# Kernel optimization log

Hardware: AMD Instinct MI355X
Metric: run time of the kernel (lower is better)

The kernel has to match this reference:

```python
import jax, jax.numpy as jnp
import numpy as np


def setup_inputs() -> dict:
    key = jax.random.key(0)
    k1, k2, k3 = jax.random.split(key, 3)
    B, C = 8192, 10000
    inp = jax.random.normal(k1, (B, C), dtype=jnp.float32)
    distance_matrix = jax.random.uniform(k2, (C, C), dtype=jnp.float32)
    target = jax.random.randint(k3, (B,), 0, C, dtype=jnp.int64)
    return {"input": inp, "distance_matrix": distance_matrix, "target": target}


def reference(input, distance_matrix, target):
    B = input.shape[0]
    C = distance_matrix.shape[0]
    # vectorized replacement for the per-sample narrow+cat loop: row gather
    distance_vector = distance_matrix[target]  # [B, C]
    # NOTE: original uses log_softmax over dim=0 (batch dim) here — faithful.
    log_sm_batch = jax.nn.log_softmax(input, axis=0)  # [B, C]
    inclusive_reg = -0.5 * jnp.sum(distance_vector * log_sm_batch) / (C * B)
    # standard cross entropy (softmax over class dim, mean over batch)
    log_sm_cls = jax.nn.log_softmax(input, axis=1)  # [B, C]
    ce = -jnp.mean(jnp.take_along_axis(log_sm_cls, target[:, None], axis=1))
    return ce + inclusive_reg
```

## Files before the change

### kernel.cpp

```cpp
#include <hip/hip_runtime.h>

#define B_DIM 8192
#define C_DIM 10000
#define C4    2500
#define NT    10
#define TILE4 256
#define NCHUNK 128
#define ROWCHUNK (B_DIM / NCHUNK)
#define NCH2  32

typedef float v4f __attribute__((ext_vector_type(4)));

__global__ __launch_bounds__(256) void fused_main(
    const v4f* __restrict__ x4, const v4f* __restrict__ dm4,
    const int* __restrict__ target,
    v4f* __restrict__ colExpPart, v4f* __restrict__ colDPart,
    float* __restrict__ rowPartExp, float* __restrict__ rowPartDx,
    float* __restrict__ xt) {
    const int tile  = blockIdx.x;
    const int chunk = blockIdx.y;
    const int tid   = threadIdx.x;
    const int lane  = tid & 63;
    const int wave  = tid >> 6;
    const int base4 = tile * TILE4;
    const int row0  = chunk * ROWCHUNK;

    __shared__ int s_t[ROWCHUNK];
    __shared__ v4f sE[TILE4];
    __shared__ v4f sD[TILE4];

    for (int r = tid; r < ROWCHUNK; r += 256) s_t[r] = target[row0 + r];
    __syncthreads();

    int  col4[4];
    bool valid[4];
    v4f accE[4], accD[4];
#pragma unroll
    for (int it = 0; it < 4; ++it) {
        col4[it]  = base4 + it * 64 + lane;
        valid[it] = col4[it] < C4;
        accE[it] = (v4f){0.f, 0.f, 0.f, 0.f};
        accD[it] = (v4f){0.f, 0.f, 0.f, 0.f};
    }

    for (int r = wave; r < ROWCHUNK; r += 4) {
        const int row = row0 + r;
        const int t   = s_t[r];
        const v4f* xrow = x4 + (size_t)row * C4;
        const v4f* drow = dm4 + (size_t)t * C4;
        const int tq = t >> 2, tl = t & 3;
        float rowE = 0.f, rowDx = 0.f;
#pragma unroll
        for (int it = 0; it < 4; ++it) {
            if (!valid[it]) continue;
            v4f xv = __builtin_nontemporal_load(&xrow[col4[it]]);
            v4f dv = drow[col4[it]];
            float ex = __expf(xv.x), ey = __expf(xv.y),
                  ez = __expf(xv.z), ew = __expf(xv.w);
            accE[it].x += ex; accE[it].y += ey; accE[it].z += ez; accE[it].w += ew;
            rowE += (ex + ey) + (ez + ew);
            accD[it].x += dv.x; accD[it].y += dv.y;
            accD[it].z += dv.z; accD[it].w += dv.w;
            rowDx += dv.x * xv.x + dv.y * xv.y + dv.z * xv.z + dv.w * xv.w;
            if (col4[it] == tq) {
                float v = (tl == 0) ? xv.x : (tl == 1) ? xv.y
                        : (tl == 2) ? xv.z : xv.w;
                xt[row] = v;
            }
        }
#pragma unroll
        for (int off = 32; off > 0; off >>= 1) {
            rowE  += __shfl_down(rowE, off, 64);
            rowDx += __shfl_down(rowDx, off, 64);
        }
        if (lane == 0) {
            rowPartExp[(size_t)tile * B_DIM + row] = rowE;
            rowPartDx [(size_t)tile * B_DIM + row] = rowDx;
        }
    }

    if (wave == 0) {
#pragma unroll
        for (int it = 0; it < 4; ++it) {
            sE[it * 64 + lane] = accE[it];
            sD[it * 64 + lane] = accD[it];
        }
    }
    __syncthreads();
    for (int w = 1; w < 4; ++w) {
        if (wave == w) {
#pragma unroll
            for (int it = 0; it < 4; ++it) {
                sE[it * 64 + lane] += accE[it];
                sD[it * 64 + lane] += accD[it];
            }
        }
        __syncthreads();
    }
    const int colg = base4 + tid;
    if (colg < C4) {
        colExpPart[(size_t)chunk * C4 + colg] = sE[tid];
        colDPart [(size_t)chunk * C4 + colg] = sD[tid];
    }
}

__global__ __launch_bounds__(256) void col_reduce1(
    const v4f* __restrict__ colExpPart, const v4f* __restrict__ colDPart,
    v4f* __restrict__ colExp2, v4f* __restrict__ colD2) {
    const int col4 = blockIdx.x * 256 + threadIdx.x;
    const int part = blockIdx.y;
    if (col4 >= C4) return;
    const int per = NCHUNK / NCH2;
    const int c0  = part * per;
    v4f se = {0.f, 0.f, 0.f, 0.f};
    v4f sd = {0.f, 0.f, 0.f, 0.f};
    for (int c = c0; c < c0 + per; ++c) {
        se += __builtin_nontemporal_load(&colExpPart[(size_t)c * C4 + col4]);
        sd += __builtin_nontemporal_load(&colDPart [(size_t)c * C4 + col4]);
    }
    colExp2[(size_t)part * C4 + col4] = se;
    colD2 [(size_t)part * C4 + col4] = sd;
}

__global__ __launch_bounds__(256) void col_finalize(
    const v4f* __restrict__ colExp2, const v4f* __restrict__ colD2,
    double* __restrict__ term2_part) {
    const int col4 = blockIdx.x * 256 + threadIdx.x;
    double t2 = 0.0;
    if (col4 < C4) {
        v4f se = {0.f, 0.f, 0.f, 0.f};
        v4f sd = {0.f, 0.f, 0.f, 0.f};
        for (int c = 0; c < NCH2; ++c) {
            se += colExp2[(size_t)c * C4 + col4];
            sd += colD2 [(size_t)c * C4 + col4];
        }
        t2 = (double)sd.x * (double)__logf(se.x)
           + (double)sd.y * (double)__logf(se.y)
           + (double)sd.z * (double)__logf(se.z)
           + (double)sd.w * (double)__logf(se.w);
    }
    __shared__ double sdd[256];
    sdd[threadIdx.x] = t2;
    __syncthreads();
    for (int s = 128; s > 0; s >>= 1) {
        if (threadIdx.x < s) sdd[threadIdx.x] += sdd[threadIdx.x + s];
        __syncthreads();
    }
    if (threadIdx.x == 0) term2_part[blockIdx.x] = sdd[0];
}

__global__ __launch_bounds__(256) void row_finalize(
    const float* __restrict__ rowPartExp, const float* __restrict__ rowPartDx,
    const float* __restrict__ xt, double* __restrict__ rowRed) {
    const int i = blockIdx.x * 256 + threadIdx.x;
    float re = 0.f, rdx = 0.f;
#pragma unroll
    for (int t = 0; t < NT; ++t) {
        re  += rowPartExp[(size_t)t * B_DIM + i];
        rdx += rowPartDx [(size_t)t * B_DIM + i];
    }
    double ce = (double)(__logf(re) - xt[i]);
    double dx = (double)rdx;
    __shared__ double s0[256], s1[256];
    s0[threadIdx.x] = ce; s1[threadIdx.x] = dx;
    __syncthreads();
    for (int s = 128; s > 0; s >>= 1) {
        if (threadIdx.x < s) {
            s0[threadIdx.x] += s0[threadIdx.x + s];
            s1[threadIdx.x] += s1[threadIdx.x + s];
        }
        __syncthreads();
    }
    if (threadIdx.x == 0) {
        rowRed[blockIdx.x * 2]     = s0[0];
        rowRed[blockIdx.x * 2 + 1] = s1[0];
    }
}

__global__ void final_k(const double* __restrict__ rowRed,
                        const double* __restrict__ term2_part,
                        float* __restrict__ out) {
    if (threadIdx.x == 0) {
        double ce = 0.0, dx = 0.0, t2 = 0.0;
        for (int b = 0; b < 32; ++b) { ce += rowRed[2 * b]; dx += rowRed[2 * b + 1]; }
        for (int b = 0; b < NT; ++b) t2 += term2_part[b];
        double ce_mean = ce / (double)B_DIM;
        double reg = -0.5 * (dx - t2) / ((double)C_DIM * (double)B_DIM);
        out[0] = (float)(ce_mean + reg);
    }
}

extern "C" void kernel_launch(void* const* d_in, const int* in_sizes, int n_in,
                              void* d_out, int out_size, void* d_ws, size_t ws_size,
                              hipStream_t stream) {
    const v4f* x4  = (const v4f*)d_in[0];
    const v4f* dm4 = (const v4f*)d_in[1];
    const int* target = (const int*)d_in[2];
    float* out = (float*)d_out;

    char* p = (char*)d_ws;
    auto alloc = [&](size_t bytes) {
        void* r = (void*)p;
        p += (bytes + 15) & ~(size_t)15;
        return r;
    };
    v4f*    colExpPart = (v4f*)alloc((size_t)NCHUNK * C4 * 16);
    v4f*    colDPart   = (v4f*)alloc((size_t)NCHUNK * C4 * 16);
    v4f*    colExp2    = (v4f*)alloc((size_t)NCH2 * C4 * 16);
    v4f*    colD2      = (v4f*)alloc((size_t)NCH2 * C4 * 16);
    float*  rowPartExp = (float*)alloc((size_t)NT * B_DIM * 4);
    float*  rowPartDx  = (float*)alloc((size_t)NT * B_DIM * 4);
    float*  xt         = (float*)alloc((size_t)B_DIM * 4);
    double* term2_part = (double*)alloc(NT * 8);
    double* rowRed     = (double*)alloc(64 * 8);

    fused_main<<<dim3(NT, NCHUNK), 256, 0, stream>>>(
        x4, dm4, target, colExpPart, colDPart, rowPartExp, rowPartDx, xt);
    col_reduce1<<<dim3(10, NCH2), 256, 0, stream>>>(
        colExpPart, colDPart, colExp2, colD2);
    col_finalize<<<10, 256, 0, stream>>>(colExp2, colD2, term2_part);
    row_finalize<<<32, 256, 0, stream>>>(rowPartExp, rowPartDx, xt, rowRed);
    final_k<<<1, 64, 0, stream>>>(rowRed, term2_part, out);
}
```

Measured before the change: 115.7 us.

## Halve row chunks and merge column and row finalize kernels into one launch

Result: slower. 118.0 us (+2.0%).

```diff
diff --git a/kernel.cpp b/kernel.cpp
--- a/kernel.cpp
+++ b/kernel.cpp
@@ -5,9 +5,9 @@
 #define C4    2500
 #define NT    10
 #define TILE4 256
-#define NCHUNK 128
+#define NCHUNK 64
 #define ROWCHUNK (B_DIM / NCHUNK)
-#define NCH2  32
+#define NCH2  16
 
 typedef float v4f __attribute__((ext_vector_type(4)));
 
@@ -104,7 +104,7 @@
     }
 }
 
-__global__ __launch_bounds__(256) void col_reduce1(
+__global__ __launch_bounds__(256) void col_reduceA(
     const v4f* __restrict__ colExpPart, const v4f* __restrict__ colDPart,
     v4f* __restrict__ colExp2, v4f* __restrict__ colD2) {
     const int col4 = blockIdx.x * 256 + threadIdx.x;
@@ -122,68 +122,73 @@
     colD2 [(size_t)part * C4 + col4] = sd;
 }
 
-__global__ __launch_bounds__(256) void col_finalize(
+__global__ __launch_bounds__(256) void fin_kernel(
     const v4f* __restrict__ colExp2, const v4f* __restrict__ colD2,
-    double* __restrict__ term2_part) {
-    const int col4 = blockIdx.x * 256 + threadIdx.x;
-    double t2 = 0.0;
-    if (col4 < C4) {
+    const float* __restrict__ rowPartExp, const float* __restrict__ rowPartDx,
+    const float* __restrict__ xt, double* __restrict__ partials) {
+    const int b   = blockIdx.x;
+    const int tid = threadIdx.x;
+    __shared__ double sred[256];
+    double mine = 0.0, mine2 = 0.0;
+
+    if (b < 40) {
+        const int col4 = b * 64 + (tid >> 2);
+        const int sub  = tid & 3;
         v4f se = {0.f, 0.f, 0.f, 0.f};
         v4f sd = {0.f, 0.f, 0.f, 0.f};
-        for (int c = 0; c < NCH2; ++c) {
-            se += colExp2[(size_t)c * C4 + col4];
-            sd += colD2 [(size_t)c * C4 + col4];
-        }
-        t2 = (double)sd.x * (double)__logf(se.x)
-           + (double)sd.y * (double)__logf(se.y)
-           + (double)sd.z * (double)__logf(se.z)
-           + (double)sd.w * (double)__logf(se.w);
-    }
-    __shared__ double sdd[256];
-    sdd[threadIdx.x] = t2;
-    __syncthreads();
-    for (int s = 128; s > 0; s >>= 1) {
-        if (threadIdx.x < s) sdd[threadIdx.x] += sdd[threadIdx.x + s];
-        __syncthreads();
-    }
-    if (threadIdx.x == 0) term2_part[blockIdx.x] = sdd[0];
-}
-
-__global__ __launch_bounds__(256) void row_finalize(
-    const float* __restrict__ rowPartExp, const float* __restrict__ rowPartDx,
-    const float* __restrict__ xt, double* __restrict__ rowRed) {
-    const int i = blockIdx.x * 256 + threadIdx.x;
-    float re = 0.f, rdx = 0.f;
-#pragma unroll
-    for (int t = 0; t < NT; ++t) {
-        re  += rowPartExp[(size_t)t * B_DIM + i];
-        rdx += rowPartDx [(size_t)t * B_DIM + i];
-    }
-    double ce = (double)(__logf(re) - xt[i]);
-    double dx = (double)rdx;
-    __shared__ double s0[256], s1[256];
-    s0[threadIdx.x] = ce; s1[threadIdx.x] = dx;
-    __syncthreads();
-    for (int s = 128; s > 0; s >>= 1) {
-        if (threadIdx.x < s) {
-            s0[threadIdx.x] += s0[threadIdx.x + s];
-            s1[threadIdx.x] += s1[threadIdx.x + s];
-        }
-        __syncthreads();
-    }
+        if (col4 < C4) {
+            for (int c = sub; c < NCH2; c += 4) {
+                se += colExp2[(size_t)c * C4 + col4];
+                sd += colD2 [(size_t)c * C4 + col4];
+            }
+        }
+        __shared__ v4f lE[256], lD[256];
+        lE[tid] = se; lD[tid] = sd;
+        __syncthreads();
+        if (sub == 0 && col4 < C4) {
+            v4f e = lE[tid] + lE[tid + 1] + lE[tid + 2] + lE[tid + 3];
+            v4f d = lD[tid] + lD[tid + 1] + lD[tid + 2] + lD[tid + 3];
+            mine = (double)d.x * (double)__logf(e.x)
+                 + (double)d.y * (double)__logf(e.y)
+                 + (double)d.z * (double)__logf(e.z)
+                 + (double)d.w * (double)__logf(e.w);
+        }
+        sred[tid] = mine;
+        __syncthreads();
+        for (int s = 128; s > 0; s >>= 1) {
+            if (tid < s) sred[tid] += sred[tid + s];
+            __syncthreads();
+        }
+        if (tid == 0) partials[b] = sred[0];
+    } else {
+        const int s = b - 40;
+        const int i = s * 256 + tid;
+        float re = 0.f, rdx = 0.f;
+#pragma unroll
+        for (int t = 0; t < NT; ++t) {
+            re  += rowPartExp[(size_t)t * B_DIM + i];
+            rdx += rowPartDx [(size_t)t * B_DIM + i];
+        }
+        mine  = (double)(__logf(re) - xt[i]);
+        mine2 = (double)rdx;
+        __shared__ double sred2[256];
+        sred[tid] = mine; sred2[tid] = mine2;
+        __syncthreads();
+        for (int st = 128; st > 0; st >>= 1) {
+            if (tid < st) { sred[tid] += sred[tid + st]; sred2[tid] += sred2[tid + st]; }
+            __syncthreads();
+        }
+        if (tid == 0) { partials[40 + s] = sred[0]; partials[72 + s] = sred2[0]; }
+    }
+}
+
+__global__ void out_kernel(const double* __restrict__ partials,
+                           float* __restrict__ out) {
     if (threadIdx.x == 0) {
-        rowRed[blockIdx.x * 2]     = s0[0];
-        rowRed[blockIdx.x * 2 + 1] = s1[0];
-    }
-}
-
-__global__ void final_k(const double* __restrict__ rowRed,
-                        const double* __restrict__ term2_part,
-                        float* __restrict__ out) {
-    if (threadIdx.x == 0) {
-        double ce = 0.0, dx = 0.0, t2 = 0.0;
-        for (int b = 0; b < 32; ++b) { ce += rowRed[2 * b]; dx += rowRed[2 * b + 1]; }
-        for (int b = 0; b < NT; ++b) t2 += term2_part[b];
+        double t2 = 0.0, ce = 0.0, dx = 0.0;
+        for (int b = 0; b < 40; ++b) t2 += partials[b];
+        for (int b = 0; b < 32; ++b) ce += partials[40 + b];
+        for (int b = 0; b < 32; ++b) dx += partials[72 + b];
         double ce_mean = ce / (double)B_DIM;
         double reg = -0.5 * (dx - t2) / ((double)C_DIM * (double)B_DIM);
         out[0] = (float)(ce_mean + reg);
@@ -211,14 +216,13 @@
     float*  rowPartExp = (float*)alloc((size_t)NT * B_DIM * 4);
     float*  rowPartDx  = (float*)alloc((size_t)NT * B_DIM * 4);
     float*  xt         = (float*)alloc((size_t)B_DIM * 4);
-    double* term2_part = (double*)alloc(NT * 8);
-    double* rowRed     = (double*)alloc(64 * 8);
+    double* partials   = (double*)alloc(104 * 8);
 
     fused_main<<<dim3(NT, NCHUNK), 256, 0, stream>>>(
         x4, dm4, target, colExpPart, colDPart, rowPartExp, rowPartDx, xt);
-    col_reduce1<<<dim3(10, NCH2), 256, 0, stream>>>(
+    col_reduceA<<<dim3(10, NCH2), 256, 0, stream>>>(
         colExpPart, colDPart, colExp2, colD2);
-    col_finalize<<<10, 256, 0, stream>>>(colExp2, colD2, term2_part);
-    row_finalize<<<32, 256, 0, stream>>>(rowPartExp, rowPartDx, xt, rowRed);
-    final_k<<<1, 64, 0, stream>>>(rowRed, term2_part, out);
-}
+    fin_kernel<<<72, 256, 0, stream>>>(
+        colExp2, colD2, rowPartExp, rowPartDx, xt, partials);
+    out_kernel<<<1, 64, 0, stream>>>(partials, out);
+}
```
